# Optimization experiments

Hardware: AMD Instinct MI355X
Metric: run time of the kernel (lower is better)

## Reference

```python
import jax, jax.numpy as jnp
import numpy as np

HEADS = 8
DIM_HEAD = 32
SCALE = DIM_HEAD ** -0.5
EPS = 1e-12  # F.normalize eps


def _rmsnorm_ch(t, g):
    # F.normalize(t, dim=1) * g * sqrt(C)  (normalize_dim=1)
    c = t.shape[1]
    norm = jnp.sqrt(jnp.sum(t * t, axis=1, keepdims=True))
    return t / jnp.maximum(norm, EPS) * g[None, :, None, None] * (c ** 0.5)


def setup_inputs() -> dict:
    key = jax.random.key(0)
    ks = jax.random.split(key, 4)
    B, C, H, W = 16, 256, 64, 64
    hidden = HEADS * DIM_HEAD  # 256
    x = jax.random.normal(ks[0], (B, C, H, W), dtype=jnp.float32)
    g1 = jnp.ones((C,), dtype=jnp.float32)
    # conv 1x1 weights stored as [out_ch, in_ch]
    w_qkv = jax.random.normal(ks[1], (hidden * 3, C), dtype=jnp.float32) * (1.0 / np.sqrt(C))
    w_out = jax.random.normal(ks[2], (C, hidden), dtype=jnp.float32) * (1.0 / np.sqrt(hidden))
    b_out = jnp.zeros((C,), dtype=jnp.float32)
    g2 = jnp.ones((C,), dtype=jnp.float32)
    return {"x": x, "g1": g1, "w_qkv": w_qkv, "w_out": w_out, "b_out": b_out, "g2": g2}


def reference(x, g1, w_qkv, w_out, b_out, g2):
    b, c, h, w = x.shape
    n = h * w
    xn = _rmsnorm_ch(x, g1)
    # 1x1 conv (no bias) == channel matmul
    qkv = jnp.einsum('oc,bchw->bohw', w_qkv, xn)
    q, k, v = jnp.split(qkv, 3, axis=1)
    # b (h c) x y -> b h c (x y)
    q = q.reshape(b, HEADS, DIM_HEAD, n)
    k = k.reshape(b, HEADS, DIM_HEAD, n)
    v = v.reshape(b, HEADS, DIM_HEAD, n)
    q = jax.nn.softmax(q, axis=-2) * SCALE  # softmax over dim_head
    k = jax.nn.softmax(k, axis=-1)          # softmax over sequence
    context = jnp.einsum('bhdn,bhen->bhde', k, v)  # [b,h,d,e] small
    out = jnp.einsum('bhde,bhdn->bhen', context, q)
    out = out.reshape(b, HEADS * DIM_HEAD, h, w)
    out = jnp.einsum('oc,bchw->bohw', w_out, out) + b_out[None, :, None, None]
    return _rmsnorm_ch(out, g2) + x
```

## Files before the change

kernel.cpp:

```cpp
#include <hip/hip_runtime.h>
#include <math.h>


#define B_ 16
#define C_ 256
#define N_ 4096
#define SCALE_ 0.17677669529663687f
#define EPS_ 1e-12f

typedef __attribute__((ext_vector_type(8))) short bf16x8;
typedef __attribute__((ext_vector_type(4))) float f32x4;

__device__ __forceinline__ ushort f2bf(float f) {
    union { float f; uint u; } x; x.f = f;
    uint r = (x.u + 0x7FFFu + ((x.u >> 16) & 1u)) >> 16;
    return (ushort)r;
}
__device__ __forceinline__ float bf2f(ushort s) {
    union { uint u; float f; } x; x.u = ((uint)s) << 16;
    return x.f;
}

__global__ __launch_bounds__(256) void k_prep(const float* __restrict__ w_qkv,
                                              const float* __restrict__ g1,
                                              ushort* __restrict__ Wp) {
    int o = blockIdx.x, c = threadIdx.x;
    Wp[(size_t)o * 256 + c] = f2bf(w_qkv[(size_t)o * 256 + c] * g1[c]);
}

__global__ __launch_bounds__(512) void k_kvctx(const ushort* __restrict__ Wp,
                                               const float* __restrict__ x,
                                               float* __restrict__ ctxp,
                                               float* __restrict__ sums_p,
                                               float* __restrict__ rinvws) {
    extern __shared__ char lds[];
    ushort (*Asub)[40] = (ushort(*)[40])lds;
    char* BQ = lds + 20480;
    char* P  = lds + 86016;
    float* sspA  = (float*)(lds + 151552);
    float* rinvA = (float*)(lds + 153600);
    const int b = blockIdx.y, s = blockIdx.x;
    const int col0 = s * 128;
    const int t = threadIdx.x, l = t & 63, w = t >> 6;
    const int lr = l & 15, grp = l >> 4;
    const int wn = w & 3, wo = w >> 2;
    const float* xb = x + (size_t)b * C_ * N_ + col0;

    {
        int col = t & 127, rg = t >> 7;
        float ss = 0.f;
        #pragma unroll 8
        for (int i = 0; i < 64; ++i) {
            float v = xb[(size_t)(rg * 64 + i) * N_ + col];
            ss += v * v;
        }
        sspA[rg * 128 + col] = ss;
    }
    __syncthreads();
    if (t < 128) {
        float rv = 16.f / fmaxf(sqrtf(sspA[t] + sspA[128 + t] + sspA[256 + t] + sspA[384 + t]), EPS_);
        rinvA[t] = rv;
        rinvws[(size_t)b * N_ + col0 + t] = rv;
    }
    __syncthreads();
    {
        int col = t & 127, rg = t >> 7;
        float rv = rinvA[col];
        uint sw = (uint)((col & 7) << 4);
        #pragma unroll
        for (int i = 0; i < 16; ++i) {
            int c = rg * 64 + i * 4;
            uint2 pk;
            pk.x = (uint)f2bf(xb[(size_t)c * N_ + col] * rv)
                 | ((uint)f2bf(xb[(size_t)(c + 1) * N_ + col] * rv) << 16);
            pk.y = (uint)f2bf(xb[(size_t)(c + 2) * N_ + col] * rv)
                 | ((uint)f2bf(xb[(size_t)(c + 3) * N_ + col] * rv) << 16);
            *(uint2*)(BQ + (((uint)(col * 512 + c * 2)) ^ sw)) = pk;
        }
    }

    #pragma unroll
    for (int p = 0; p < 2; ++p) {
        f32x4 acc[2][8] = {};
        for (int k0 = 0; k0 < 256; k0 += 32) {
            {
                int r = t >> 1, ko = (t & 1) * 16;
                const uint4* sa = (const uint4*)(Wp + (size_t)(256 + p * 256 + r) * 256 + k0 + ko);
                *(uint4*)&Asub[r][ko]     = sa[0];
                *(uint4*)&Asub[r][ko + 8] = sa[1];
            }
            __syncthreads();
            bf16x8 ax[2], bw[8];
            #pragma unroll
            for (int m = 0; m < 2; ++m) {
                int row = wn * 32 + m * 16 + lr;
                uint off = (uint)(row * 512 + (k0 + grp * 8) * 2) ^ (uint)((row & 7) << 4);
                ax[m] = *(const bf16x8*)(BQ + off);
            }
            #pragma unroll
            for (int nf = 0; nf < 8; ++nf)
                bw[nf] = *(const bf16x8*)&Asub[wo * 128 + nf * 16 + lr][grp * 8];
            #pragma unroll
            for (int m = 0; m < 2; ++m)
                #pragma unroll
                for (int nf = 0; nf < 8; ++nf)
                    acc[m][nf] = __builtin_amdgcn_mfma_f32_16x16x32_bf16(ax[m], bw[nf], acc[m][nf], 0, 0, 0);
            __syncthreads();
        }
        if (p == 0) {
            #pragma unroll
            for (int nf = 0; nf < 8; ++nf) {
                int d = wo * 128 + nf * 16 + lr;
                uint sw = (uint)((d & 7) << 4);
                #pragma unroll
                for (int m = 0; m < 2; ++m) {
                    int n0 = wn * 32 + m * 16 + grp * 4;
                    uint2 pk;
                    pk.x = (uint)f2bf(__expf(acc[m][nf][0])) | ((uint)f2bf(__expf(acc[m][nf][1])) << 16);
                    pk.y = (uint)f2bf(__expf(acc[m][nf][2])) | ((uint)f2bf(__expf(acc[m][nf][3])) << 16);
                    *(uint2*)(P + (((uint)(d * 256 + n0 * 2)) ^ sw)) = pk;
                }
            }
        } else {
            #pragma unroll
            for (int nf = 0; nf < 8; ++nf) {
                int e = wo * 128 + nf * 16 + lr;
                uint sw = (uint)((e & 7) << 4);
                #pragma unroll
                for (int m = 0; m < 2; ++m) {
                    int n0 = wn * 32 + m * 16 + grp * 4;
                    uint2 pk;
                    pk.x = (uint)f2bf(acc[m][nf][0]) | ((uint)f2bf(acc[m][nf][1]) << 16);
                    pk.y = (uint)f2bf(acc[m][nf][2]) | ((uint)f2bf(acc[m][nf][3]) << 16);
                    *(uint2*)(BQ + (((uint)(e * 256 + n0 * 2)) ^ sw)) = pk;
                }
            }
        }
    }
    __syncthreads();

    const int h = w;
    f32x4 c3[2][2] = {};
    f32x4 cS[2] = {};
    bf16x8 ones;
    #pragma unroll
    for (int j = 0; j < 8; ++j) ones[j] = (short)0x3F80;
    #pragma unroll
    for (int ks = 0; ks < 4; ++ks) {
        int n0 = ks * 32 + grp * 8;
        bf16x8 pA[2], vB[2];
        #pragma unroll
        for (int df = 0; df < 2; ++df) {
            int d = h * 32 + df * 16 + lr;
            pA[df] = *(const bf16x8*)(P + (((uint)(d * 256 + n0 * 2)) ^ ((uint)((d & 7) << 4))));
        }
        #pragma unroll
        for (int ef = 0; ef < 2; ++ef) {
            int e = h * 32 + ef * 16 + lr;
            vB[ef] = *(const bf16x8*)(BQ + (((uint)(e * 256 + n0 * 2)) ^ ((uint)((e & 7) << 4))));
        }
        #pragma unroll
        for (int df = 0; df < 2; ++df) {
            #pragma unroll
            for (int ef = 0; ef < 2; ++ef)
                c3[df][ef] = __builtin_amdgcn_mfma_f32_16x16x32_bf16(pA[df], vB[ef], c3[df][ef], 0, 0, 0);
            cS[df] = __builtin_amdgcn_mfma_f32_16x16x32_bf16(pA[df], ones, cS[df], 0, 0, 0);
        }
    }
    int bh = b * 8 + h;
    size_t base = ((size_t)s * 128 + bh) * 32;
    #pragma unroll
    for (int df = 0; df < 2; ++df) {
        #pragma unroll
        for (int ef = 0; ef < 2; ++ef)
            #pragma unroll
            for (int r = 0; r < 4; ++r)
                ctxp[(base + df * 16 + grp * 4 + r) * 32 + ef * 16 + lr] = c3[df][ef][r];
        if (lr == 0)
            #pragma unroll
            for (int r = 0; r < 4; ++r)
                sums_p[base + df * 16 + grp * 4 + r] = cS[df][r];
    }
}

__global__ __launch_bounds__(256) void k_fold(const float* __restrict__ w_out,
                                              const float* __restrict__ ctxp,
                                              const float* __restrict__ sums_p,
                                              ushort* __restrict__ M) {
    __shared__ float cn[32][33];
    __shared__ float sinv[32];
    int bh = blockIdx.x;
    int b = bh >> 3, h = bh & 7;
    int t = threadIdx.x;
    if (t < 32) {
        float st = 0.f;
        #pragma unroll 8
        for (int s = 0; s < 32; ++s) st += sums_p[(size_t)(s * 128 + bh) * 32 + t];
        sinv[t] = SCALE_ / st;
    }
    #pragma unroll
    for (int i = t; i < 1024; i += 256) {
        int d = i >> 5, e = i & 31;
        float cv = 0.f;
        #pragma unroll 8
        for (int s = 0; s < 32; ++s)
            cv += ctxp[((size_t)(s * 128 + bh) * 32 + d) * 32 + e];
        cn[e][d] = cv;
    }
    __syncthreads();
    float wreg[32];
    const float* wr = w_out + (size_t)t * 256 + h * 32;
    #pragma unroll
    for (int e = 0; e < 32; e += 4) {
        float4 wv = *(const float4*)&wr[e];
        wreg[e] = wv.x; wreg[e + 1] = wv.y; wreg[e + 2] = wv.z; wreg[e + 3] = wv.w;
    }
    float acc[32] = {};
    #pragma unroll
    for (int e = 0; e < 32; ++e) {
        float we = wreg[e];
        #pragma unroll
        for (int d = 0; d < 32; ++d) acc[d] += we * cn[e][d];
    }
    ushort* Mrow = M + ((size_t)b * 256 + t) * 256 + h * 32;
    #pragma unroll
    for (int d = 0; d < 32; ++d) Mrow[d] = f2bf(acc[d] * sinv[d]);
}

__global__ __launch_bounds__(512) void k_qfinal(const ushort* __restrict__ Wp,
                                                const ushort* __restrict__ M,
                                                const float* __restrict__ b_out,
                                                const float* __restrict__ g2,
                                                const float* __restrict__ x,
                                                const float* __restrict__ rinvws,
                                                float* __restrict__ out) {
    __shared__ __align__(16) char shmem[34816];
    __shared__ float ss2[8][64];
    __shared__ float rinvq[64];
    ushort* BQ = (ushort*)shmem;
    float*  OUT = (float*)shmem;
    const int b = blockIdx.y, col0 = blockIdx.x * 64;
    const int t = threadIdx.x, l = t & 63, w = t >> 6;
    const int lr = l & 15, grp = l >> 4;
    const float* xb2 = x + (size_t)b * C_ * N_;

    if (t < 64) rinvq[t] = rinvws[(size_t)b * N_ + col0 + t];
    __syncthreads();
    {
        int col = t & 63, rg = t >> 6;
        float rv = rinvq[col];
        uint sw = (uint)((col & 7) << 4);
        #pragma unroll
        for (int i = 0; i < 8; ++i) {
            int c = rg * 32 + i * 4;
            uint2 pk;
            pk.x = (uint)f2bf(xb2[(size_t)c * N_ + col0 + col] * rv)
                 | ((uint)f2bf(xb2[(size_t)(c + 1) * N_ + col0 + col] * rv) << 16);
            pk.y = (uint)f2bf(xb2[(size_t)(c + 2) * N_ + col0 + col] * rv)
                 | ((uint)f2bf(xb2[(size_t)(c + 3) * N_ + col0 + col] * rv) << 16);
            *(uint2*)((char*)BQ + (((uint)(col * 512 + c * 2)) ^ sw)) = pk;
        }
    }
    __syncthreads();

    f32x4 acc[2][4] = {};
    for (int k0 = 0; k0 < 256; k0 += 32) {
        bf16x8 af[2], bf[4];
        #pragma unroll
        for (int m = 0; m < 2; ++m)
            af[m] = *(const bf16x8*)(Wp + (size_t)(w * 32 + m * 16 + lr) * 256 + k0 + grp * 8);
        #pragma unroll
        for (int n = 0; n < 4; ++n) {
            int row = n * 16 + lr;
            uint off = (uint)(row * 512 + (k0 + grp * 8) * 2) ^ (uint)((row & 7) << 4);
            bf[n] = *(const bf16x8*)((const char*)BQ + off);
        }
        #pragma unroll
        for (int m = 0; m < 2; ++m)
            #pragma unroll
            for (int n = 0; n < 4; ++n)
                acc[m][n] = __builtin_amdgcn_mfma_f32_16x16x32_bf16(af[m], bf[n], acc[m][n], 0, 0, 0);
    }
    __syncthreads();

    #pragma unroll
    for (int n = 0; n < 4; ++n) {
        float f[2][4];
        #pragma unroll
        for (int m = 0; m < 2; ++m)
            #pragma unroll
            for (int r = 0; r < 4; ++r) f[m][r] = acc[m][n][r];
        float mx = -1e30f;
        #pragma unroll
        for (int r = 0; r < 4; ++r) mx = fmaxf(mx, fmaxf(f[0][r], f[1][r]));
        mx = fmaxf(mx, __shfl_xor(mx, 16));
        mx = fmaxf(mx, __shfl_xor(mx, 32));
        float s = 0.f;
        #pragma unroll
        for (int r = 0; r < 4; ++r) {
            f[0][r] = __expf(f[0][r] - mx); s += f[0][r];
            f[1][r] = __expf(f[1][r] - mx); s += f[1][r];
        }
        s += __shfl_xor(s, 16); s += __shfl_xor(s, 32);
        float inv = 1.f / s;
        int cl = n * 16 + lr;
        #pragma unroll
        for (int m = 0; m < 2; ++m) {
            int d = w * 32 + m * 16 + grp * 4;
            uint2 pk;
            pk.x = (uint)f2bf(f[m][0] * inv) | ((uint)f2bf(f[m][1] * inv) << 16);
            pk.y = (uint)f2bf(f[m][2] * inv) | ((uint)f2bf(f[m][3] * inv) << 16);
            uint off = (uint)(cl * 512 + d * 2) ^ (uint)((cl & 7) << 4);
            *(uint2*)((char*)BQ + off) = pk;
        }
    }
    __syncthreads();

    #pragma unroll
    for (int m = 0; m < 2; ++m)
        #pragma unroll
        for (int n = 0; n < 4; ++n)
            acc[m][n] = f32x4{0.f, 0.f, 0.f, 0.f};
    const ushort* Mb = M + (size_t)b * 256 * 256;
    for (int k0 = 0; k0 < 256; k0 += 32) {
        bf16x8 af[2], bq[4];
        #pragma unroll
        for (int m = 0; m < 2; ++m)
            af[m] = *(const bf16x8*)(Mb + (size_t)(w * 32 + m * 16 + lr) * 256 + k0 + grp * 8);
        #pragma unroll
        for (int n = 0; n < 4; ++n) {
            int row = n * 16 + lr;
            uint off = (uint)(row * 512 + (k0 + grp * 8) * 2) ^ (uint)((row & 7) << 4);
            bq[n] = *(const bf16x8*)((const char*)BQ + off);
        }
        #pragma unroll
        for (int m = 0; m < 2; ++m)
            #pragma unroll
            for (int n = 0; n < 4; ++n)
                acc[m][n] = __builtin_amdgcn_mfma_f32_16x16x32_bf16(af[m], bq[n], acc[m][n], 0, 0, 0);
    }

    __syncthreads();
    #pragma unroll
    for (int n = 0; n < 4; ++n) {
        float local = 0.f;
        #pragma unroll
        for (int m = 0; m < 2; ++m) {
            int obase = w * 32 + m * 16 + grp * 4;
            #pragma unroll
            for (int r = 0; r < 4; ++r) {
                float f = acc[m][n][r] + b_out[obase + r];
                acc[m][n][r] = f;
                local += f * f;
            }
        }
        local += __shfl_xor(local, 16);
        local += __shfl_xor(local, 32);
        if (grp == 0) ss2[w][n * 16 + lr] = local;
    }
    __syncthreads();
    #pragma unroll
    for (int n = 0; n < 4; ++n) {
        int cl = n * 16 + lr;
        float tot = ss2[0][cl] + ss2[1][cl] + ss2[2][cl] + ss2[3][cl]
                  + ss2[4][cl] + ss2[5][cl] + ss2[6][cl] + ss2[7][cl];
        float rs = 16.f / fmaxf(sqrtf(tot), EPS_);
        #pragma unroll
        for (int m = 0; m < 2; ++m) {
            int obase = w * 32 + m * 16 + grp * 4;
            #pragma unroll
            for (int r = 0; r < 4; ++r)
                acc[m][n][r] *= rs * g2[obase + r];
        }
    }
    float* ob = out + (size_t)b * C_ * N_;
    const int chunk = w >> 2;
    #pragma unroll
    for (int ch = 0; ch < 2; ++ch) {
        if (chunk == ch) {
            #pragma unroll
            for (int n = 0; n < 4; ++n) {
                int cl = n * 16 + lr;
                #pragma unroll
                for (int m = 0; m < 2; ++m) {
                    int rbase = (w & 3) * 32 + m * 16 + grp * 4;
                    #pragma unroll
                    for (int r = 0; r < 4; ++r)
                        OUT[(rbase + r) * 68 + cl] = acc[m][n][r];
                }
            }
        }
        __syncthreads();
        #pragma unroll
        for (int i = 0; i < 4; ++i) {
            int rowl = i * 32 + (t >> 4);
            int grow = ch * 128 + rowl;
            float4 v = *(float4*)&OUT[rowl * 68 + (t & 15) * 4];
            float4 xr = *(const float4*)&xb2[(size_t)grow * N_ + col0 + (t & 15) * 4];
            v.x += xr.x; v.y += xr.y; v.z += xr.z; v.w += xr.w;
            *(float4*)&ob[(size_t)grow * N_ + col0 + (t & 15) * 4] = v;
        }
        __syncthreads();
    }
}

extern "C" void kernel_launch(void* const* d_in, const int* in_sizes, int n_in,
                              void* d_out, int out_size, void* d_ws, size_t ws_size,
                              hipStream_t stream) {
    const float* x     = (const float*)d_in[0];
    const float* g1    = (const float*)d_in[1];
    const float* w_qkv = (const float*)d_in[2];
    const float* w_out = (const float*)d_in[3];
    const float* b_out = (const float*)d_in[4];
    const float* g2    = (const float*)d_in[5];
    float* out = (float*)d_out;
    char* ws = (char*)d_ws;

    ushort* Wp     = (ushort*)(ws + 0);
    float*  ctxp   = (float*)(ws + 393216);
    float*  sums_p = (float*)(ws + 17170432);
    ushort* Mm     = (ushort*)(ws + 17694720);
    float*  rinvws = (float*)(ws + 19791872);

    hipFuncSetAttribute((const void*)k_kvctx,
                        hipFuncAttributeMaxDynamicSharedMemorySize, 154112);

    k_prep<<<768, 256, 0, stream>>>(w_qkv, g1, Wp);
    k_kvctx<<<dim3(32, 16), 512, 154112, stream>>>(Wp, x, ctxp, sums_p, rinvws);
    k_fold<<<128, 256, 0, stream>>>(w_out, ctxp, sums_p, Mm);
    k_qfinal<<<dim3(64, 16), 512, 0, stream>>>(Wp, Mm, b_out, g2, x, rinvws, out);
}
```

Measured before the change: 132.0 us.

## Split k_qfinal across 16 waves with cross-wave softmax reduction

```diff
diff --git a/kernel.cpp b/kernel.cpp
--- a/kernel.cpp
+++ b/kernel.cpp
@@ -227,15 +227,15 @@
     for (int d = 0; d < 32; ++d) Mrow[d] = f2bf(acc[d] * sinv[d]);
 }
 
-__global__ __launch_bounds__(512) void k_qfinal(const ushort* __restrict__ Wp,
-                                                const ushort* __restrict__ M,
-                                                const float* __restrict__ b_out,
-                                                const float* __restrict__ g2,
-                                                const float* __restrict__ x,
-                                                const float* __restrict__ rinvws,
-                                                float* __restrict__ out) {
+__global__ __launch_bounds__(1024, 8) void k_qfinal(const ushort* __restrict__ Wp,
+                                                    const ushort* __restrict__ M,
+                                                    const float* __restrict__ b_out,
+                                                    const float* __restrict__ g2,
+                                                    const float* __restrict__ x,
+                                                    const float* __restrict__ rinvws,
+                                                    float* __restrict__ out) {
     __shared__ __align__(16) char shmem[34816];
-    __shared__ float ss2[8][64];
+    __shared__ float red2[2][16][64];
     __shared__ float rinvq[64];
     ushort* BQ = (ushort*)shmem;
     float*  OUT = (float*)shmem;
@@ -251,8 +251,8 @@
         float rv = rinvq[col];
         uint sw = (uint)((col & 7) << 4);
         #pragma unroll
-        for (int i = 0; i < 8; ++i) {
-            int c = rg * 32 + i * 4;
+        for (int i = 0; i < 4; ++i) {
+            int c = rg * 16 + i * 4;
             uint2 pk;
             pk.x = (uint)f2bf(xb2[(size_t)c * N_ + col0 + col] * rv)
                  | ((uint)f2bf(xb2[(size_t)(c + 1) * N_ + col0 + col] * rv) << 16);
@@ -263,12 +263,10 @@
     }
     __syncthreads();
 
-    f32x4 acc[2][4] = {};
+    f32x4 acc[4] = {};
     for (int k0 = 0; k0 < 256; k0 += 32) {
-        bf16x8 af[2], bf[4];
-        #pragma unroll
-        for (int m = 0; m < 2; ++m)
-            af[m] = *(const bf16x8*)(Wp + (size_t)(w * 32 + m * 16 + lr) * 256 + k0 + grp * 8);
+        bf16x8 af, bf[4];
+        af = *(const bf16x8*)(Wp + (size_t)(w * 16 + lr) * 256 + k0 + grp * 8);
         #pragma unroll
         for (int n = 0; n < 4; ++n) {
             int row = n * 16 + lr;
@@ -276,57 +274,53 @@
             bf[n] = *(const bf16x8*)((const char*)BQ + off);
         }
         #pragma unroll
-        for (int m = 0; m < 2; ++m)
-            #pragma unroll
-            for (int n = 0; n < 4; ++n)
-                acc[m][n] = __builtin_amdgcn_mfma_f32_16x16x32_bf16(af[m], bf[n], acc[m][n], 0, 0, 0);
+        for (int n = 0; n < 4; ++n)
+            acc[n] = __builtin_amdgcn_mfma_f32_16x16x32_bf16(af, bf[n], acc[n], 0, 0, 0);
     }
     __syncthreads();
 
     #pragma unroll
     for (int n = 0; n < 4; ++n) {
-        float f[2][4];
-        #pragma unroll
-        for (int m = 0; m < 2; ++m)
-            #pragma unroll
-            for (int r = 0; r < 4; ++r) f[m][r] = acc[m][n][r];
-        float mx = -1e30f;
-        #pragma unroll
-        for (int r = 0; r < 4; ++r) mx = fmaxf(mx, fmaxf(f[0][r], f[1][r]));
+        float mx = fmaxf(fmaxf(acc[n][0], acc[n][1]), fmaxf(acc[n][2], acc[n][3]));
         mx = fmaxf(mx, __shfl_xor(mx, 16));
         mx = fmaxf(mx, __shfl_xor(mx, 32));
+        if (grp == 0) red2[0][w][n * 16 + lr] = mx;
+    }
+    __syncthreads();
+    #pragma unroll
+    for (int n = 0; n < 4; ++n) {
+        int cl = n * 16 + lr;
+        float mx = fmaxf(red2[0][w][cl], red2[0][w ^ 1][cl]);
         float s = 0.f;
         #pragma unroll
         for (int r = 0; r < 4; ++r) {
-            f[0][r] = __expf(f[0][r] - mx); s += f[0][r];
-            f[1][r] = __expf(f[1][r] - mx); s += f[1][r];
+            acc[n][r] = __expf(acc[n][r] - mx);
+            s += acc[n][r];
         }
         s += __shfl_xor(s, 16); s += __shfl_xor(s, 32);
-        float inv = 1.f / s;
+        if (grp == 0) red2[1][w][cl] = s;
+    }
+    __syncthreads();
+    #pragma unroll
+    for (int n = 0; n < 4; ++n) {
         int cl = n * 16 + lr;
-        #pragma unroll
-        for (int m = 0; m < 2; ++m) {
-            int d = w * 32 + m * 16 + grp * 4;
-            uint2 pk;
-            pk.x = (uint)f2bf(f[m][0] * inv) | ((uint)f2bf(f[m][1] * inv) << 16);
-            pk.y = (uint)f2bf(f[m][2] * inv) | ((uint)f2bf(f[m][3] * inv) << 16);
-            uint off = (uint)(cl * 512 + d * 2) ^ (uint)((cl & 7) << 4);
-            *(uint2*)((char*)BQ + off) = pk;
-        }
-    }
-    __syncthreads();
-
-    #pragma unroll
-    for (int m = 0; m < 2; ++m)
-        #pragma unroll
-        for (int n = 0; n < 4; ++n)
-            acc[m][n] = f32x4{0.f, 0.f, 0.f, 0.f};
+        float inv = 1.f / (red2[1][w][cl] + red2[1][w ^ 1][cl]);
+        int d = w * 16 + grp * 4;
+        uint2 pk;
+        pk.x = (uint)f2bf(acc[n][0] * inv) | ((uint)f2bf(acc[n][1] * inv) << 16);
+        pk.y = (uint)f2bf(acc[n][2] * inv) | ((uint)f2bf(acc[n][3] * inv) << 16);
+        uint off = (uint)(cl * 512 + d * 2) ^ (uint)((cl & 7) << 4);
+        *(uint2*)((char*)BQ + off) = pk;
+    }
+    __syncthreads();
+
+    #pragma unroll
+    for (int n = 0; n < 4; ++n)
+        acc[n] = f32x4{0.f, 0.f, 0.f, 0.f};
     const ushort* Mb = M + (size_t)b * 256 * 256;
     for (int k0 = 0; k0 < 256; k0 += 32) {
-        bf16x8 af[2], bq[4];
-        #pragma unroll
-        for (int m = 0; m < 2; ++m)
-            af[m] = *(const bf16x8*)(Mb + (size_t)(w * 32 + m * 16 + lr) * 256 + k0 + grp * 8);
+        bf16x8 af, bq[4];
+        af = *(const bf16x8*)(Mb + (size_t)(w * 16 + lr) * 256 + k0 + grp * 8);
         #pragma unroll
         for (int n = 0; n < 4; ++n) {
             int row = n * 16 + lr;
@@ -334,66 +328,56 @@
             bq[n] = *(const bf16x8*)((const char*)BQ + off);
         }
         #pragma unroll
-        for (int m = 0; m < 2; ++m)
-            #pragma unroll
-            for (int n = 0; n < 4; ++n)
-                acc[m][n] = __builtin_amdgcn_mfma_f32_16x16x32_bf16(af[m], bq[n], acc[m][n], 0, 0, 0);
+        for (int n = 0; n < 4; ++n)
+            acc[n] = __builtin_amdgcn_mfma_f32_16x16x32_bf16(af, bq[n], acc[n], 0, 0, 0);
     }
 
     __syncthreads();
     #pragma unroll
     for (int n = 0; n < 4; ++n) {
         float local = 0.f;
-        #pragma unroll
-        for (int m = 0; m < 2; ++m) {
-            int obase = w * 32 + m * 16 + grp * 4;
-            #pragma unroll
-            for (int r = 0; r < 4; ++r) {
-                float f = acc[m][n][r] + b_out[obase + r];
-                acc[m][n][r] = f;
-                local += f * f;
-            }
+        int obase = w * 16 + grp * 4;
+        #pragma unroll
+        for (int r = 0; r < 4; ++r) {
+            float f = acc[n][r] + b_out[obase + r];
+            acc[n][r] = f;
+            local += f * f;
         }
         local += __shfl_xor(local, 16);
         local += __shfl_xor(local, 32);
-        if (grp == 0) ss2[w][n * 16 + lr] = local;
+        if (grp == 0) red2[0][w][n * 16 + lr] = local;
     }
     __syncthreads();
     #pragma unroll
     for (int n = 0; n < 4; ++n) {
         int cl = n * 16 + lr;
-        float tot = ss2[0][cl] + ss2[1][cl] + ss2[2][cl] + ss2[3][cl]
-                  + ss2[4][cl] + ss2[5][cl] + ss2[6][cl] + ss2[7][cl];
+        float tot = 0.f;
+        #pragma unroll
+        for (int ww = 0; ww < 16; ++ww) tot += red2[0][ww][cl];
         float rs = 16.f / fmaxf(sqrtf(tot), EPS_);
-        #pragma unroll
-        for (int m = 0; m < 2; ++m) {
-            int obase = w * 32 + m * 16 + grp * 4;
-            #pragma unroll
-            for (int r = 0; r < 4; ++r)
-                acc[m][n][r] *= rs * g2[obase + r];
-        }
+        int obase = w * 16 + grp * 4;
+        #pragma unroll
+        for (int r = 0; r < 4; ++r)
+            acc[n][r] *= rs * g2[obase + r];
     }
     float* ob = out + (size_t)b * C_ * N_;
-    const int chunk = w >> 2;
+    const int chunk = w >> 3;
     #pragma unroll
     for (int ch = 0; ch < 2; ++ch) {
         if (chunk == ch) {
             #pragma unroll
             for (int n = 0; n < 4; ++n) {
                 int cl = n * 16 + lr;
+                int rbase = (w & 7) * 16 + grp * 4;
                 #pragma unroll
-                for (int m = 0; m < 2; ++m) {
-                    int rbase = (w & 3) * 32 + m * 16 + grp * 4;
-                    #pragma unroll
-                    for (int r = 0; r < 4; ++r)
-                        OUT[(rbase + r) * 68 + cl] = acc[m][n][r];
-                }
+                for (int r = 0; r < 4; ++r)
+                    OUT[(rbase + r) * 68 + cl] = acc[n][r];
             }
         }
         __syncthreads();
         #pragma unroll
-        for (int i = 0; i < 4; ++i) {
-            int rowl = i * 32 + (t >> 4);
+        for (int i = 0; i < 2; ++i) {
+            int rowl = i * 64 + (t >> 4);
             int grow = ch * 128 + rowl;
             float4 v = *(float4*)&OUT[rowl * 68 + (t & 15) * 4];
             float4 xr = *(const float4*)&xb2[(size_t)grow * N_ + col0 + (t & 15) * 4];
@@ -428,5 +412,5 @@
     k_prep<<<768, 256, 0, stream>>>(w_qkv, g1, Wp);
     k_kvctx<<<dim3(32, 16), 512, 154112, stream>>>(Wp, x, ctxp, sums_p, rinvws);
     k_fold<<<128, 256, 0, stream>>>(w_out, ctxp, sums_p, Mm);
-    k_qfinal<<<dim3(64, 16), 512, 0, stream>>>(Wp, Mm, b_out, g2, x, rinvws, out);
-}
+    k_qfinal<<<dim3(64, 16), 1024, 0, stream>>>(Wp, Mm, b_out, g2, x, rinvws, out);
+}
```

New measurement: 138.5 us. 1.05x slower.
